# Performance work log

Hardware: AMD Instinct MI355X
Metric: run time of the kernel (lower is better)

The kernel has to match this reference:

```python
import jax, jax.numpy as jnp
import numpy as np

EPSILON = 1e-15
CUTOFF = 5.0
N_RBF = 16           # num_radial_filters -> RBF dim = 2*16+1 = 33
SCALE = 8            # _quadrature_points_per_atom_scaling


def poly_envelope_5_2(x):
    # e3nn.poly_envelope(5, 2): f'(x) ~ x^5 (1-x)^2, f(0)=1, f(1)=0
    x2 = x * x
    x6 = x2 * x2 * x2
    f = 1.0 - 28.0 * x6 + 48.0 * x6 * x - 21.0 * x6 * x2
    return jnp.where(x < 1.0, f, jnp.zeros_like(x))


def sin_cos_basis(r, n_rbf):
    r = r[..., None]                                  # [A,T,1]
    k = jnp.arange(1, n_rbf + 1, dtype=r.dtype)       # [n_rbf]
    return jnp.sqrt(2.0) * jnp.concatenate(
        [0.1 * jnp.ones_like(r), jnp.sin(k * jnp.pi * r), jnp.cos(k * jnp.pi * r)],
        axis=-1,
    )                                                 # [A,T,2*n_rbf+1]


def spherical_harmonics_l012_norm(d):
    # Real spherical harmonics up to l=2, e3nn m-ordering, normalization='norm'
    # (each l-block has unit norm for unit input directions).
    x, y, z = d[..., 0], d[..., 1], d[..., 2]
    r2 = x * x + y * y + z * z
    s3 = jnp.sqrt(3.0)
    one = jnp.ones_like(x)
    return jnp.stack(
        [
            one,                       # l=0
            y, z, x,                   # l=1 (m=-1,0,1)
            s3 * x * y,                # l=2 m=-2
            s3 * y * z,                # l=2 m=-1
            0.5 * (3.0 * z * z - r2),  # l=2 m=0
            s3 * x * z,                # l=2 m=1
            0.5 * s3 * (x * x - y * y) # l=2 m=2
        ],
        axis=-1,
    )                                  # [A,T,9]


def setup_inputs() -> dict:
    key = jax.random.key(0)
    k1, k2, k3, k4 = jax.random.split(key, 4)
    A, N = 64, 200000
    nuc_pos = 4.0 * jax.random.normal(k1, (A, 3), dtype=jnp.float32)
    grid_coords = 4.0 * jax.random.normal(k2, (N, 3), dtype=jnp.float32)
    weights = jax.random.uniform(k3, (N,), dtype=jnp.float32)
    n = jax.random.uniform(k4, (N,), dtype=jnp.float32)
    atom_mask = jnp.ones((A,), dtype=bool)
    return {"nuc_pos": nuc_pos, "atom_mask": atom_mask,
            "grid_coords": grid_coords, "weights": weights, "n": n}


def reference(nuc_pos, atom_mask, grid_coords, weights, n):
    g = grid_coords / CUTOFF                          # [N,3]
    p = nuc_pos / CUTOFF                              # [A,3]
    diff = p[:, None] - g[None]                       # [A,N,3]
    dist = jnp.linalg.norm(diff, axis=-1)             # [A,N]
    A, N = dist.shape
    T = min(N, SCALE * N // A)                        # static
    idx = jnp.argsort(dist, axis=1)[:, :T]            # [A,T] nearest grid points
    diff = jnp.take_along_axis(diff, idx[:, :, None], axis=1)   # [A,T,3]
    dist = jnp.take_along_axis(dist, idx, axis=1)                # [A,T]
    n_t = n[idx]                                      # [A,T]
    w_t = weights[idx]                                # [A,T]
    rbf = sin_cos_basis(dist, N_RBF) * poly_envelope_5_2(dist)[..., None]  # [A,T,33]
    dirs = diff / (dist[..., None] + EPSILON)         # [A,T,3]
    sh = spherical_harmonics_l012_norm(dirs)          # [A,T,9]
    node_feats = jnp.einsum('atr,ath,at,at->arh', rbf, sh, n_t, w_t)  # [A,33,9]
    return node_feats
```

## Files before the change

kernel.cpp:

```cpp
#include <hip/hip_runtime.h>
#include <hip/hip_fp16.h>


typedef float f32x4 __attribute__((ext_vector_type(4)));
typedef int   i32x4 __attribute__((ext_vector_type(4)));

#define SLICES 32
#define NB1    256
#define NB2    512
#define CLAMP0 4000u
#define NCHUNK SLICES
#define PBSTR  304
#define CUT25  0x41C80000u
#define WROWS  49
#define BBASE  (33 * 72)

__device__ __forceinline__ unsigned short tobf(float v) {
  return (unsigned short)((__float_as_uint(v) + 0x8000u) >> 16);
}

__device__ __forceinline__ unsigned pack2h(float a, float b) {
  __half2 h = __floats2half2_rn(a, b);
  return *reinterpret_cast<unsigned*>(&h);
}

__device__ __forceinline__ void mfma_acc(f32x4& d, i32x4 a, i32x4 b) {
  asm("v_mfma_f32_16x16x32_bf16 %0, %1, %2, %0" : "+v"(d) : "v"(a), "v"(b));
}

__global__ __launch_bounds__(256) void enc_hist_store(
    const float* __restrict__ nuc, const float* __restrict__ grid,
    const float* __restrict__ wv, const float* __restrict__ nv, int N,
    unsigned* __restrict__ hists, unsigned* __restrict__ cnt,
    unsigned* __restrict__ bitsArr, uint2* __restrict__ pay, int scap,
    unsigned* __restrict__ ghist2) {
  __shared__ unsigned lh[NB1];
  __shared__ unsigned s_cnt;
  int a = blockIdx.x / SLICES, s = blockIdx.x % SLICES;
  int tid = threadIdx.x, lane = tid & 63;
  if (tid < NB1) lh[tid] = 0;
  if (tid == 0) s_cnt = 0;
  {
    const int stripe = NB2 / SLICES;
    if (tid < stripe) ghist2[(size_t)a * NB2 + s * stripe + tid] = 0;
  }
  __syncthreads();

  float px = nuc[3*a+0], py = nuc[3*a+1], pz = nuc[3*a+2];
  unsigned* segb = bitsArr + (size_t)blockIdx.x * scap;
  uint2*    segp = pay     + (size_t)blockIdx.x * scap;
  const float4* G4 = (const float4*)grid;
  const float4* W4 = (const float4*)wv;
  const float4* V4 = (const float4*)nv;
  int nq = N >> 2;
  int qper = (nq + SLICES - 1) / SLICES;
  int qlo = s * qper, qhi = min(nq, qlo + qper);

  for (int qb = qlo; qb < qhi; qb += 256) {
    int qi = qb + tid;
    bool qv = qi < qhi;
    float dxs[4], dys[4], dzs[4], nws[4];
    unsigned bt[4];
    if (qv) {
      float4 A4 = G4[3*qi], B4 = G4[3*qi+1], C4 = G4[3*qi+2];
      float4 w4 = W4[qi], v4 = V4[qi];
      float xs[4] = {A4.x, A4.w, B4.z, C4.y};
      float ys[4] = {A4.y, B4.x, B4.w, C4.z};
      float zs[4] = {A4.z, B4.y, C4.x, C4.w};
      nws[0] = v4.x * w4.x; nws[1] = v4.y * w4.y;
      nws[2] = v4.z * w4.z; nws[3] = v4.w * w4.w;
      #pragma unroll
      for (int k = 0; k < 4; ++k) {
        float dx = px - xs[k], dy = py - ys[k], dz = pz - zs[k];
        dxs[k] = dx; dys[k] = dy; dzs[k] = dz;
        float d2 = __fmaf_rn(dx, dx, __fmaf_rn(dy, dy, __fmul_rn(dz, dz)));
        bt[k] = __float_as_uint(d2);
        if (bt[k] < CUT25) {
          int cb = (int)(bt[k] >> 18) - (int)CLAMP0;
          atomicAdd(&lh[cb > 0 ? cb : 0], 1u);
        }
      }
    } else {
      #pragma unroll
      for (int k = 0; k < 4; ++k) bt[k] = 0xFFFFFFFFu;
    }
    unsigned csel = 0;
    #pragma unroll
    for (int k = 0; k < 4; ++k) csel += (bt[k] < CUT25) ? 1u : 0u;
    unsigned p = csel;
    #pragma unroll
    for (int d = 1; d < 64; d <<= 1) {
      unsigned t = __shfl_up(p, d);
      if (lane >= d) p += t;
    }
    unsigned wtot = __shfl(p, 63);
    unsigned excl = p - csel;
    unsigned base = 0;
    if (wtot) {
      if (lane == 0) base = atomicAdd(&s_cnt, wtot);
      base = __shfl(base, 0);
      unsigned pos = base + excl;
      #pragma unroll
      for (int k = 0; k < 4; ++k) {
        if (bt[k] < CUT25) {
          if (pos < (unsigned)scap) {
            segb[pos] = bt[k];
            segp[pos] = make_uint2(pack2h(dxs[k], dys[k]), pack2h(dzs[k], nws[k]));
          }
          ++pos;
        }
      }
    }
  }
  if (s == SLICES - 1) {
    for (int i = 4*nq + tid; i < N; i += 256) {
      float dx = px - grid[3*i+0], dy = py - grid[3*i+1], dz = pz - grid[3*i+2];
      float d2 = __fmaf_rn(dx, dx, __fmaf_rn(dy, dy, __fmul_rn(dz, dz)));
      unsigned bits = __float_as_uint(d2);
      bool sel = bits < CUT25;
      if (sel) {
        int cb = (int)(bits >> 18) - (int)CLAMP0;
        atomicAdd(&lh[cb > 0 ? cb : 0], 1u);
      }
      unsigned long long mm = __ballot(sel);
      if (mm) {
        int leader = __ffsll(mm) - 1;
        unsigned base = 0;
        if (lane == leader) base = atomicAdd(&s_cnt, (unsigned)__popcll(mm));
        base = __shfl(base, leader);
        if (sel) {
          unsigned pos = base + (unsigned)__popcll(mm & ((1ull << lane) - 1ull));
          if (pos < (unsigned)scap) {
            segb[pos] = bits;
            segp[pos] = make_uint2(pack2h(dx, dy), pack2h(dz, nv[i] * wv[i]));
          }
        }
      }
    }
  }
  __syncthreads();
  if (tid < NB1) hists[(size_t)blockIdx.x * NB1 + tid] = lh[tid];
  if (tid == 0) cnt[blockIdx.x] = s_cnt;
}

__global__ __launch_bounds__(256) void enc_scan1(
    const unsigned* __restrict__ hists, unsigned T,
    unsigned* __restrict__ b1r, unsigned* __restrict__ r2r) {
  __shared__ unsigned lh[NB1];
  __shared__ unsigned s_bin, s_pre;
  int a = blockIdx.x, tid = threadIdx.x;
  if (tid < NB1) {
    unsigned acc = 0;
    const unsigned* base = hists + (size_t)a * SLICES * NB1 + tid;
    #pragma unroll 8
    for (int t = 0; t < SLICES; ++t) acc += base[(size_t)t * NB1];
    lh[tid] = acc;
  }
  if (tid == 0) { s_bin = NB1 - 1; s_pre = 0; }
  __syncthreads();
  if (tid < 64) {
    int lane = tid, base = 4 * lane;
    unsigned h0 = lh[base], h1 = lh[base+1], h2 = lh[base+2], h3 = lh[base+3];
    unsigned ssum = h0 + h1 + h2 + h3;
    unsigned p = ssum;
    #pragma unroll
    for (int d = 1; d < 64; d <<= 1) {
      unsigned t = __shfl_up(p, d);
      if (lane >= d) p += t;
    }
    unsigned excl = p - ssum;
    if (excl < T && T <= p) {
      unsigned cum = excl;
      unsigned hh[4] = {h0, h1, h2, h3};
      #pragma unroll
      for (int k = 0; k < 4; ++k) {
        if (cum + hh[k] >= T) { s_bin = (unsigned)(base + k); s_pre = cum; break; }
        cum += hh[k];
      }
    }
  }
  __syncthreads();
  if (tid == 0) { b1r[a] = s_bin; r2r[a] = T - s_pre; }
}

__global__ __launch_bounds__(256) void enc_fine(
    const unsigned* __restrict__ b1r, const unsigned* __restrict__ cnt,
    const unsigned* __restrict__ bitsArr, int scap,
    unsigned* __restrict__ ghist2) {
  int seg_id = blockIdx.x;
  int a = seg_id / SLICES;
  unsigned b1c = b1r[a];
  unsigned tb1 = b1c + CLAMP0;
  int total = min((int)cnt[seg_id], scap);
  const unsigned* segb = bitsArr + (size_t)seg_id * scap;
  unsigned* gh2 = ghist2 + (size_t)a * NB2;
  for (int i = threadIdx.x; i < total; i += 256) {
    unsigned bits = segb[i];
    unsigned cb = bits >> 18;
    bool match = b1c ? (cb == tb1) : (cb <= CLAMP0);
    if (match) atomicAdd(&gh2[(bits >> 9) & (NB2 - 1)], 1u);
  }
}

__global__ __launch_bounds__(256) void enc_scan2(
    const unsigned* __restrict__ ghist2, const unsigned* __restrict__ b1r,
    const unsigned* __restrict__ r2r, unsigned* __restrict__ thr) {
  __shared__ unsigned lh2[NB2];
  __shared__ unsigned s_bin2;
  int a = blockIdx.x, tid = threadIdx.x;
  const unsigned* gh2 = ghist2 + (size_t)a * NB2;
  lh2[tid] = gh2[tid];
  lh2[tid + 256] = gh2[tid + 256];
  if (tid == 0) s_bin2 = NB2 - 1;
  __syncthreads();
  unsigned R = r2r[a];
  if (tid < 64) {
    int lane = tid, base = 8 * lane;
    unsigned hh[8], ssum = 0;
    #pragma unroll
    for (int k = 0; k < 8; ++k) { hh[k] = lh2[base + k]; ssum += hh[k]; }
    unsigned p = ssum;
    #pragma unroll
    for (int d = 1; d < 64; d <<= 1) {
      unsigned t = __shfl_up(p, d);
      if (lane >= d) p += t;
    }
    unsigned excl = p - ssum;
    if (excl < R && R <= p) {
      unsigned cum = excl;
      #pragma unroll
      for (int k = 0; k < 8; ++k) {
        if (cum + hh[k] >= R) { s_bin2 = (unsigned)(base + k); break; }
        cum += hh[k];
      }
    }
  }
  __syncthreads();
  if (tid == 0) thr[a] = ((b1r[a] + CLAMP0) << 9) | s_bin2;
}

__global__ __launch_bounds__(256, 5) void enc_accum(
    const unsigned* __restrict__ thrv, const unsigned* __restrict__ cnt,
    const unsigned* __restrict__ bitsArr, const uint2* __restrict__ pay,
    int scap, float* __restrict__ pb) {
  __shared__ __align__(16) unsigned short lds[4][WROWS * 72];
  int seg_id = blockIdx.x;
  int a = seg_id / SLICES;
  int tid = threadIdx.x, lane = tid & 63, w = tid >> 6;
  unsigned short* SB = &lds[w][0];

  {
    i32x4 z = {0, 0, 0, 0};
    i32x4* zp = (i32x4*)SB;
    #pragma unroll
    for (int t = 0; t < 7; ++t) {
      int idx = lane + t * 64;
      if (idx < (WROWS * 72) / 8) zp[idx] = z;
    }
  }

  unsigned thr = thrv[a];
  int total = min((int)cnt[seg_id], scap);
  const unsigned* lstb = bitsArr + (size_t)seg_id * scap;
  const uint2*    lstp = pay     + (size_t)seg_id * scap;

  f32x4 acc0 = {0,0,0,0}, acc1 = {0,0,0,0}, acc2 = {0,0,0,0};
  int m = lane & 15, q = lane >> 4;
  const float SQRT2 = 1.41421356237309515f;
  const float PIF   = 3.14159265358979323846f;
  const float S3    = 1.73205080756887729f;

  int j0 = w * 64 + lane;
  unsigned bitsN = (j0 < total) ? lstb[j0] : 0xFFFFFFFFu;
  uint2 prN = make_uint2(0u, 0u);
  if (j0 < total) prN = lstp[j0];

  for (int jb = w * 64; jb < total; jb += 256) {
    unsigned bits = bitsN;
    uint2 pr = prN;
    int jn = jb + 256 + lane;
    if (jn < total) { bitsN = lstb[jn]; prN = lstp[jn]; }
    bool live = (jb + lane < total) && ((bits >> 9) <= thr);
    if (live) {
      float d2 = __uint_as_float(bits);
      __half2 hxy = *reinterpret_cast<const __half2*>(&pr.x);
      __half2 hzn = *reinterpret_cast<const __half2*>(&pr.y);
      float dx = __low2float(hxy), dy = __high2float(hxy);
      float dz = __low2float(hzn), nw = __high2float(hzn);
#if __has_builtin(__builtin_amdgcn_sqrtf)
      float rn = __builtin_amdgcn_sqrtf(d2) * 0.2f;
#else
      float rn = sqrtf(d2) * 0.2f;
#endif
      float x2 = rn * rn;
      float x6 = x2 * x2 * x2;
      float e  = __fmaf_rn(x6, __fmaf_rn(-21.f, x2, __fmaf_rn(48.f, rn, -28.f)), 1.f);
      float f  = SQRT2 * e;
#if __has_builtin(__builtin_amdgcn_rcpf)
      float inv = 0.2f * __builtin_amdgcn_rcpf(rn + 1e-15f);
#else
      float inv = 0.2f / (rn + 1e-15f);
#endif
      float X = dx * inv, Y = dy * inv, Z = dz * inv;
      float r2 = __fmaf_rn(X, X, __fmaf_rn(Y, Y, Z * Z));
      SB[BBASE + 0*72 + lane] = tobf(nw);
      SB[BBASE + 1*72 + lane] = tobf(nw * Y);
      SB[BBASE + 2*72 + lane] = tobf(nw * Z);
      SB[BBASE + 3*72 + lane] = tobf(nw * X);
      SB[BBASE + 4*72 + lane] = tobf(nw * S3 * X * Y);
      SB[BBASE + 5*72 + lane] = tobf(nw * S3 * Y * Z);
      SB[BBASE + 6*72 + lane] = tobf(nw * 0.5f * __fmaf_rn(3.f, Z * Z, -r2));
      SB[BBASE + 7*72 + lane] = tobf(nw * S3 * X * Z);
      SB[BBASE + 8*72 + lane] = tobf(nw * 0.5f * S3 * (X * X - Y * Y));
      float s1, c1;
      __sincosf(PIF * rn, &s1, &c1);
      SB[0 * 72 + lane]  = tobf(0.1f * f);
      float sk = s1, ck = c1;
      SB[1 * 72 + lane]  = tobf(f * sk);
      SB[17 * 72 + lane] = tobf(f * ck);
      #pragma unroll
      for (int k = 2; k <= 16; ++k) {
        float sn = __fmaf_rn(sk, c1, ck * s1);
        float cn = __fmaf_rn(ck, c1, -(sk * s1));
        sk = sn; ck = cn;
        SB[k * 72 + lane]        = tobf(f * sk);
        SB[(16 + k) * 72 + lane] = tobf(f * ck);
      }
    } else {
      #pragma unroll
      for (int h = 0; h < 9; ++h) SB[BBASE + h * 72 + lane] = 0;
    }
    #pragma unroll
    for (int g = 0; g < 2; ++g) {
      int cb = 8 * q + 32 * g;
      i32x4 bf = *(const i32x4*)&SB[BBASE + m * 72 + cb];
      i32x4 a0 = *(const i32x4*)&SB[(0  + m) * 72 + cb];
      mfma_acc(acc0, a0, bf);
      i32x4 a1 = *(const i32x4*)&SB[(16 + m) * 72 + cb];
      mfma_acc(acc1, a1, bf);
      i32x4 a2 = *(const i32x4*)&SB[(32 + m) * 72 + cb];
      mfma_acc(acc2, a2, bf);
    }
  }
  asm volatile("s_nop 7\n\ts_nop 7" : "+v"(acc0), "+v"(acc1), "+v"(acc2));

  float* redw = (float*)&lds[w][0];
  if (m < 9) {
    #pragma unroll
    for (int t = 0; t < 4; ++t) {
      int row = 4 * q + t;
      redw[(row +  0) * 9 + m] = acc0[t];
      redw[(row + 16) * 9 + m] = acc1[t];
      if (row + 32 < 33) redw[(row + 32) * 9 + m] = acc2[t];
    }
  }
  __syncthreads();
  float* pbb = pb + (size_t)blockIdx.x * PBSTR;
  for (int v = tid; v < 297; v += 256) {
    float s0 = ((const float*)&lds[0][0])[v] + ((const float*)&lds[1][0])[v];
    float s1 = ((const float*)&lds[2][0])[v] + ((const float*)&lds[3][0])[v];
    pbb[v] = s0 + s1;
  }
}

__global__ __launch_bounds__(256) void enc_reduce(
    const float* __restrict__ pb, float* __restrict__ out, int nout) {
  int idx = blockIdx.x * 256 + threadIdx.x;
  if (idx >= nout) return;
  int a = idx / 297, v = idx - a * 297;
  const float* p = pb + (size_t)a * NCHUNK * PBSTR + v;
  float s = 0.f;
  #pragma unroll 8
  for (int k = 0; k < NCHUNK; ++k) s += p[(size_t)k * PBSTR];
  out[idx] = s;
}

extern "C" void kernel_launch(void* const* d_in, const int* in_sizes, int n_in,
                              void* d_out, int out_size, void* d_ws, size_t ws_size,
                              hipStream_t stream) {
  const float* nuc  = (const float*)d_in[0];
  const float* grid = (const float*)d_in[2];
  const float* wts  = (const float*)d_in[3];
  const float* nn   = (const float*)d_in[4];
  int A = in_sizes[0] / 3;
  int N = in_sizes[2] / 3;
  long long t8 = (8LL * (long long)N) / (long long)A;
  unsigned T = (unsigned)(t8 < (long long)N ? t8 : (long long)N);

  unsigned* ws      = (unsigned*)d_ws;
  unsigned* cnt     = ws;
  unsigned* b1r     = cnt + A * SLICES;
  unsigned* r2r     = b1r + A;
  unsigned* thr     = r2r + A;
  unsigned* hists   = thr + A;
  unsigned* ghist2  = hists + (size_t)A * SLICES * NB1;
  float*    pb      = (float*)(ghist2 + (size_t)A * NB2);
  unsigned* bitsArr = (unsigned*)(pb + (size_t)A * NCHUNK * PBSTR);

  int nq   = N >> 2;
  int qper = (nq + SLICES - 1) / SLICES;
  int SCAP = qper * 4 + 4;
  {
    long long head  = (long long)(bitsArr - ws);
    long long avail = (long long)(ws_size / 4) - head;
    long long need  = 3LL * SCAP * A * SLICES;
    if (avail > 0 && need > avail) SCAP = (int)(avail / (3LL * A * SLICES));
    SCAP &= ~1;
  }
  uint2* pay = (uint2*)(bitsArr + (size_t)A * SLICES * SCAP);
  float* out = (float*)d_out;
  int nout = A * 297;

  enc_hist_store<<<A * SLICES,         256, 0, stream>>>(nuc, grid, wts, nn, N, hists,
                                                         cnt, bitsArr, pay, SCAP, ghist2);
  enc_scan1     <<<A,                  256, 0, stream>>>(hists, T, b1r, r2r);
  enc_fine      <<<A * SLICES,         256, 0, stream>>>(b1r, cnt, bitsArr, SCAP, ghist2);
  enc_scan2     <<<A,                  256, 0, stream>>>(ghist2, b1r, r2r, thr);
  enc_accum     <<<A * SLICES,         256, 0, stream>>>(thr, cnt, bitsArr, pay, SCAP, pb);
  enc_reduce    <<<(nout + 255) / 256, 256, 0, stream>>>(pb, out, nout);
}
```

Baseline: 57.45 us.

## Process two points per lane in enc_accum with packed bf16 LDS stores

Each lane now handles two consecutive list entries per iteration, using wider vector loads for bits and payload and packing the two results into one bf16x2 LDS store with v_cvt_pk_bf16_f32. The LDS tile stride grows to 136 so each wave's MFMA step covers 128 points (four K-groups instead of two). Dead entries become branchless masked zeros instead of a divergent branch. The larger LDS footprint and register use lower the occupancy hint from 5 to 3 waves per SIMD, which could reduce latency hiding.

```diff
diff --git a/kernel.cpp b/kernel.cpp
--- a/kernel.cpp
+++ b/kernel.cpp
@@ -13,7 +13,8 @@
 #define PBSTR  304
 #define CUT25  0x41C80000u
 #define WROWS  49
-#define BBASE  (33 * 72)
+#define CSTR   136
+#define CSTRD  (CSTR / 2)
 
 __device__ __forceinline__ unsigned short tobf(float v) {
   return (unsigned short)((__float_as_uint(v) + 0x8000u) >> 16);
@@ -22,6 +23,12 @@
 __device__ __forceinline__ unsigned pack2h(float a, float b) {
   __half2 h = __floats2half2_rn(a, b);
   return *reinterpret_cast<unsigned*>(&h);
+}
+
+__device__ __forceinline__ unsigned pkbf(float a, float b) {
+  unsigned r;
+  asm("v_cvt_pk_bf16_f32 %0, %1, %2" : "=v"(r) : "v"(a), "v"(b));
+  return r;
 }
 
 __device__ __forceinline__ void mfma_acc(f32x4& d, i32x4 a, i32x4 b) {
@@ -239,23 +246,24 @@
   if (tid == 0) thr[a] = ((b1r[a] + CLAMP0) << 9) | s_bin2;
 }
 
-__global__ __launch_bounds__(256, 5) void enc_accum(
+__global__ __launch_bounds__(256, 3) void enc_accum(
     const unsigned* __restrict__ thrv, const unsigned* __restrict__ cnt,
     const unsigned* __restrict__ bitsArr, const uint2* __restrict__ pay,
     int scap, float* __restrict__ pb) {
-  __shared__ __align__(16) unsigned short lds[4][WROWS * 72];
+  __shared__ __align__(16) unsigned short lds[4][WROWS * CSTR];
   int seg_id = blockIdx.x;
   int a = seg_id / SLICES;
   int tid = threadIdx.x, lane = tid & 63, w = tid >> 6;
   unsigned short* SB = &lds[w][0];
+  unsigned* SBd = (unsigned*)SB;
 
   {
     i32x4 z = {0, 0, 0, 0};
     i32x4* zp = (i32x4*)SB;
     #pragma unroll
-    for (int t = 0; t < 7; ++t) {
+    for (int t = 0; t < 14; ++t) {
       int idx = lane + t * 64;
-      if (idx < (WROWS * 72) / 8) zp[idx] = z;
+      if (idx < (WROWS * CSTR) / 8) zp[idx] = z;
     }
   }
 
@@ -270,75 +278,102 @@
   const float PIF   = 3.14159265358979323846f;
   const float S3    = 1.73205080756887729f;
 
-  int j0 = w * 64 + lane;
-  unsigned bitsN = (j0 < total) ? lstb[j0] : 0xFFFFFFFFu;
-  uint2 prN = make_uint2(0u, 0u);
-  if (j0 < total) prN = lstp[j0];
-
-  for (int jb = w * 64; jb < total; jb += 256) {
-    unsigned bits = bitsN;
-    uint2 pr = prN;
-    int jn = jb + 256 + lane;
-    if (jn < total) { bitsN = lstb[jn]; prN = lstp[jn]; }
-    bool live = (jb + lane < total) && ((bits >> 9) <= thr);
-    if (live) {
-      float d2 = __uint_as_float(bits);
-      __half2 hxy = *reinterpret_cast<const __half2*>(&pr.x);
-      __half2 hzn = *reinterpret_cast<const __half2*>(&pr.y);
-      float dx = __low2float(hxy), dy = __high2float(hxy);
-      float dz = __low2float(hzn), nw = __high2float(hzn);
+  int jp = w * 128 + 2 * lane;
+  uint2 b2N = make_uint2(0xFFFFFFFFu, 0xFFFFFFFFu);
+  uint4 p4N = make_uint4(0u, 0u, 0u, 0u);
+  if (jp < total) {
+    b2N = *reinterpret_cast<const uint2*>(&lstb[jp]);
+    p4N = *reinterpret_cast<const uint4*>(&lstp[jp]);
+  }
+
+  for (int jb = w * 128; jb < total; jb += 512) {
+    uint2 b2 = b2N; uint4 p4 = p4N;
+    int jn = jb + 512 + 2 * lane;
+    if (jn < total) {
+      b2N = *reinterpret_cast<const uint2*>(&lstb[jn]);
+      p4N = *reinterpret_cast<const uint4*>(&lstp[jn]);
+    }
+    int jj = jb + 2 * lane;
+    bool live0 = (jj     < total) && ((b2.x >> 9) <= thr);
+    bool live1 = (jj + 1 < total) && ((b2.y >> 9) <= thr);
+
+    float d20 = live0 ? __uint_as_float(b2.x) : 1.0f;
+    float d21 = live1 ? __uint_as_float(b2.y) : 1.0f;
+    __half2 hxy0 = *reinterpret_cast<const __half2*>(&p4.x);
+    __half2 hzn0 = *reinterpret_cast<const __half2*>(&p4.y);
+    __half2 hxy1 = *reinterpret_cast<const __half2*>(&p4.z);
+    __half2 hzn1 = *reinterpret_cast<const __half2*>(&p4.w);
+    float dx0 = live0 ? __low2float(hxy0) : 0.f;
+    float dy0 = live0 ? __high2float(hxy0) : 0.f;
+    float dz0 = live0 ? __low2float(hzn0) : 0.f;
+    float nw0 = live0 ? __high2float(hzn0) : 0.f;
+    float dx1 = live1 ? __low2float(hxy1) : 0.f;
+    float dy1 = live1 ? __high2float(hxy1) : 0.f;
+    float dz1 = live1 ? __low2float(hzn1) : 0.f;
+    float nw1 = live1 ? __high2float(hzn1) : 0.f;
+
 #if __has_builtin(__builtin_amdgcn_sqrtf)
-      float rn = __builtin_amdgcn_sqrtf(d2) * 0.2f;
+    float rn0 = __builtin_amdgcn_sqrtf(d20) * 0.2f;
+    float rn1 = __builtin_amdgcn_sqrtf(d21) * 0.2f;
 #else
-      float rn = sqrtf(d2) * 0.2f;
+    float rn0 = sqrtf(d20) * 0.2f;
+    float rn1 = sqrtf(d21) * 0.2f;
 #endif
-      float x2 = rn * rn;
-      float x6 = x2 * x2 * x2;
-      float e  = __fmaf_rn(x6, __fmaf_rn(-21.f, x2, __fmaf_rn(48.f, rn, -28.f)), 1.f);
-      float f  = SQRT2 * e;
+    float x20 = rn0 * rn0, x21 = rn1 * rn1;
+    float x60 = x20 * x20 * x20, x61 = x21 * x21 * x21;
+    float e0 = __fmaf_rn(x60, __fmaf_rn(-21.f, x20, __fmaf_rn(48.f, rn0, -28.f)), 1.f);
+    float e1 = __fmaf_rn(x61, __fmaf_rn(-21.f, x21, __fmaf_rn(48.f, rn1, -28.f)), 1.f);
+    float f0 = live0 ? SQRT2 * e0 : 0.f;
+    float f1 = live1 ? SQRT2 * e1 : 0.f;
 #if __has_builtin(__builtin_amdgcn_rcpf)
-      float inv = 0.2f * __builtin_amdgcn_rcpf(rn + 1e-15f);
+    float inv0 = 0.2f * __builtin_amdgcn_rcpf(rn0 + 1e-15f);
+    float inv1 = 0.2f * __builtin_amdgcn_rcpf(rn1 + 1e-15f);
 #else
-      float inv = 0.2f / (rn + 1e-15f);
+    float inv0 = 0.2f / (rn0 + 1e-15f);
+    float inv1 = 0.2f / (rn1 + 1e-15f);
 #endif
-      float X = dx * inv, Y = dy * inv, Z = dz * inv;
-      float r2 = __fmaf_rn(X, X, __fmaf_rn(Y, Y, Z * Z));
-      SB[BBASE + 0*72 + lane] = tobf(nw);
-      SB[BBASE + 1*72 + lane] = tobf(nw * Y);
-      SB[BBASE + 2*72 + lane] = tobf(nw * Z);
-      SB[BBASE + 3*72 + lane] = tobf(nw * X);
-      SB[BBASE + 4*72 + lane] = tobf(nw * S3 * X * Y);
-      SB[BBASE + 5*72 + lane] = tobf(nw * S3 * Y * Z);
-      SB[BBASE + 6*72 + lane] = tobf(nw * 0.5f * __fmaf_rn(3.f, Z * Z, -r2));
-      SB[BBASE + 7*72 + lane] = tobf(nw * S3 * X * Z);
-      SB[BBASE + 8*72 + lane] = tobf(nw * 0.5f * S3 * (X * X - Y * Y));
-      float s1, c1;
-      __sincosf(PIF * rn, &s1, &c1);
-      SB[0 * 72 + lane]  = tobf(0.1f * f);
-      float sk = s1, ck = c1;
-      SB[1 * 72 + lane]  = tobf(f * sk);
-      SB[17 * 72 + lane] = tobf(f * ck);
-      #pragma unroll
-      for (int k = 2; k <= 16; ++k) {
-        float sn = __fmaf_rn(sk, c1, ck * s1);
-        float cn = __fmaf_rn(ck, c1, -(sk * s1));
-        sk = sn; ck = cn;
-        SB[k * 72 + lane]        = tobf(f * sk);
-        SB[(16 + k) * 72 + lane] = tobf(f * ck);
-      }
-    } else {
-      #pragma unroll
-      for (int h = 0; h < 9; ++h) SB[BBASE + h * 72 + lane] = 0;
-    }
-    #pragma unroll
-    for (int g = 0; g < 2; ++g) {
+    float X0 = dx0 * inv0, Y0 = dy0 * inv0, Z0 = dz0 * inv0;
+    float X1 = dx1 * inv1, Y1 = dy1 * inv1, Z1 = dz1 * inv1;
+    float r20 = __fmaf_rn(X0, X0, __fmaf_rn(Y0, Y0, Z0 * Z0));
+    float r21 = __fmaf_rn(X1, X1, __fmaf_rn(Y1, Y1, Z1 * Z1));
+
+    SBd[(33+0)*CSTRD + lane] = pkbf(nw0,            nw1);
+    SBd[(33+1)*CSTRD + lane] = pkbf(nw0 * Y0,       nw1 * Y1);
+    SBd[(33+2)*CSTRD + lane] = pkbf(nw0 * Z0,       nw1 * Z1);
+    SBd[(33+3)*CSTRD + lane] = pkbf(nw0 * X0,       nw1 * X1);
+    SBd[(33+4)*CSTRD + lane] = pkbf(nw0 * S3*X0*Y0, nw1 * S3*X1*Y1);
+    SBd[(33+5)*CSTRD + lane] = pkbf(nw0 * S3*Y0*Z0, nw1 * S3*Y1*Z1);
+    SBd[(33+6)*CSTRD + lane] = pkbf(nw0 * 0.5f*__fmaf_rn(3.f, Z0*Z0, -r20),
+                                    nw1 * 0.5f*__fmaf_rn(3.f, Z1*Z1, -r21));
+    SBd[(33+7)*CSTRD + lane] = pkbf(nw0 * S3*X0*Z0, nw1 * S3*X1*Z1);
+    SBd[(33+8)*CSTRD + lane] = pkbf(nw0 * 0.5f*S3*(X0*X0 - Y0*Y0),
+                                    nw1 * 0.5f*S3*(X1*X1 - Y1*Y1));
+    float s10, c10, s11, c11;
+    __sincosf(PIF * rn0, &s10, &c10);
+    __sincosf(PIF * rn1, &s11, &c11);
+    SBd[0*CSTRD + lane]  = pkbf(0.1f * f0, 0.1f * f1);
+    float sk0 = s10, ck0 = c10, sk1 = s11, ck1 = c11;
+    SBd[1*CSTRD + lane]  = pkbf(f0 * sk0, f1 * sk1);
+    SBd[17*CSTRD + lane] = pkbf(f0 * ck0, f1 * ck1);
+    #pragma unroll
+    for (int k = 2; k <= 16; ++k) {
+      float sn0 = __fmaf_rn(sk0, c10, ck0 * s10);
+      float cn0 = __fmaf_rn(ck0, c10, -(sk0 * s10));
+      float sn1 = __fmaf_rn(sk1, c11, ck1 * s11);
+      float cn1 = __fmaf_rn(ck1, c11, -(sk1 * s11));
+      sk0 = sn0; ck0 = cn0; sk1 = sn1; ck1 = cn1;
+      SBd[k*CSTRD + lane]      = pkbf(f0 * sk0, f1 * sk1);
+      SBd[(16+k)*CSTRD + lane] = pkbf(f0 * ck0, f1 * ck1);
+    }
+    #pragma unroll
+    for (int g = 0; g < 4; ++g) {
       int cb = 8 * q + 32 * g;
-      i32x4 bf = *(const i32x4*)&SB[BBASE + m * 72 + cb];
-      i32x4 a0 = *(const i32x4*)&SB[(0  + m) * 72 + cb];
+      i32x4 bf = *(const i32x4*)&SB[(33 + m) * CSTR + cb];
+      i32x4 a0 = *(const i32x4*)&SB[(0  + m) * CSTR + cb];
       mfma_acc(acc0, a0, bf);
-      i32x4 a1 = *(const i32x4*)&SB[(16 + m) * 72 + cb];
+      i32x4 a1 = *(const i32x4*)&SB[(16 + m) * CSTR + cb];
       mfma_acc(acc1, a1, bf);
-      i32x4 a2 = *(const i32x4*)&SB[(32 + m) * 72 + cb];
+      i32x4 a2 = *(const i32x4*)&SB[(32 + m) * CSTR + cb];
       mfma_acc(acc2, a2, bf);
     }
   }
```

Result: faster. 54.90 us (-4.4%).
